# Performance work log

Measured on AMD Instinct MI355X. Metric: run time of the kernel, lower is better.

Reference implementation:

```python
import jax, jax.numpy as jnp
import numpy as np

N_NODES = 50000
N_EDGES = 1600000
DIM_IN = 128
DIM_OUT = 128
EPS = 1e-10


def setup_inputs() -> dict:
    key = jax.random.key(0)
    k1, k2, k3, k4, k5 = jax.random.split(key, 5)
    feat_in = jax.random.normal(k1, (N_NODES, DIM_IN), dtype=jnp.float32)
    rows = jax.random.randint(k2, (N_EDGES,), 0, N_NODES, dtype=jnp.int32)
    cols = jax.random.randint(k3, (N_EDGES,), 0, N_NODES, dtype=jnp.int32)
    # normalized adjacency values (positive, ~1/deg scale)
    vals = jax.random.uniform(k4, (N_EDGES,), dtype=jnp.float32) / 32.0
    W = jax.random.normal(k5, (DIM_OUT, DIM_IN), dtype=jnp.float32) * 0.05
    b = jnp.zeros((DIM_OUT,), dtype=jnp.float32)
    scale = jnp.ones((DIM_OUT,), dtype=jnp.float32)
    offset = jnp.zeros((DIM_OUT,), dtype=jnp.float32)
    return {"feat_in": feat_in, "rows": rows, "cols": cols, "vals": vals,
            "W": W, "b": b, "scale": scale, "offset": offset}


def reference(feat_in, rows, cols, vals, W, b, scale, offset):
    # torch.sparse.mm(adj_norm, feat_in): gather source features, scale by
    # edge value, scatter-add into destination rows.
    msgs = vals[:, None] * feat_in[cols]                       # [E, D_in]
    feat_aggr = jax.ops.segment_sum(msgs, rows, num_segments=N_NODES)  # [N, D_in]
    # f_lin (nn.Linear): x @ W.T + b
    feat_trans = feat_aggr @ W.T + b                           # [N, D_out]
    # act = ReLU
    a = jax.nn.relu(feat_trans)
    # f_norm: per-row (feature-dim) normalization, biased variance
    mean = jnp.mean(a, axis=1, keepdims=True)
    var = jnp.mean((a - mean) ** 2, axis=1, keepdims=True) + EPS
    feat_out = (a - mean) * scale * jax.lax.rsqrt(var) + offset
    return feat_out
```

## Files before the change

kernel.cpp:

```cpp
#include <hip/hip_runtime.h>

typedef unsigned int uint;
typedef unsigned short ushort;
typedef unsigned long long ullong;
typedef __attribute__((ext_vector_type(8))) short short8;
typedef __attribute__((ext_vector_type(4))) float floatx4;

#define N_NODES 50000
#define N_EDGES 1600000
#define DIM 128
#define LN_EPS 1e-10f

#define NB2 1564
#define CAP2 1280
#define EPB 6250
#define SB 256
#define CONVB 256
#define CAPR 76

__device__ __forceinline__ uint f2bf(float x) {
    uint u = __float_as_uint(x);
    return (u + 0x7FFFu + ((u >> 16) & 1u)) >> 16;
}

__global__ __launch_bounds__(1024, 8) void prep(
    const float* __restrict__ feat, const float* __restrict__ W,
    const int* __restrict__ rows, const int* __restrict__ cols,
    const float* __restrict__ vals, int* __restrict__ gcnt,
    int2* __restrict__ perm, uint* __restrict__ featb_u,
    ushort* __restrict__ wbf)
{
    __shared__ int  cnt[NB2];
    __shared__ int  gbase[NB2];
    __shared__ int  lbase[NB2];
    __shared__ int  csum[64];
    __shared__ int2 stageE[EPB];
    const int bx = blockIdx.x;
    const int t  = threadIdx.x;

    if (bx >= SB) {
        const int cb = bx - SB;
        const int stride = CONVB * 1024;
        for (int i = cb * 1024 + t; i < N_NODES * DIM / 4; i += stride) {
            float4 v = ((const float4*)feat)[i];
            ((uint2*)featb_u)[i] = make_uint2(
                f2bf(v.x) | (f2bf(v.y) << 16),
                f2bf(v.z) | (f2bf(v.w) << 16));
        }
        for (int i = cb * 1024 + t; i < DIM * DIM / 4; i += stride) {
            float4 v = ((const float4*)W)[i];
            ushort4 o;
            o.x = (ushort)f2bf(v.x); o.y = (ushort)f2bf(v.y);
            o.z = (ushort)f2bf(v.z); o.w = (ushort)f2bf(v.w);
            ((ushort4*)wbf)[i] = o;
        }
        return;
    }

    for (int i = t; i < NB2; i += 1024) cnt[i] = 0;
    __syncthreads();
    const int base = bx * EPB;
    uint pk[7];
    #pragma unroll
    for (int i = 0; i < 7; ++i) {
        int k = i * 1024 + t;
        if (k < EPB) {
            int r = rows[base + k];
            int rank = atomicAdd(&cnt[r >> 5], 1);
            pk[i] = ((uint)rank << 16) | (uint)r;
        }
    }
    __syncthreads();

    {
        const int rot = (bx * 16) % NB2;
        for (int i = t; i < NB2; i += 1024) {
            int ii = i + rot; if (ii >= NB2) ii -= NB2;
            int c = cnt[ii];
            gbase[ii] = c ? atomicAdd(&gcnt[ii], c) : 0;
        }
    }
    if (t < 64) {
        int s = 0;
        for (int j = 0; j < 25; ++j) {
            int idx = t * 25 + j;
            if (idx < NB2) s += cnt[idx];
        }
        csum[t] = s;
    }
    __syncthreads();
    if (t == 0) {
        int s = 0;
        for (int i = 0; i < 64; ++i) { int c = csum[i]; csum[i] = s; s += c; }
    }
    __syncthreads();
    if (t < 64) {
        int run = csum[t];
        for (int j = 0; j < 25; ++j) {
            int idx = t * 25 + j;
            if (idx < NB2) { lbase[idx] = run; run += cnt[idx]; }
        }
    }
    __syncthreads();

    #pragma unroll
    for (int i = 0; i < 7; ++i) {
        int k = i * 1024 + t;
        if (k < EPB) {
            uint s = pk[i];
            int r = (int)(s & 0xFFFFu);
            int rank = (int)(s >> 16);
            int b = r >> 5;
            int pos = lbase[b] + rank;
            stageE[pos] = make_int2(
                (uint)cols[base + k] | ((uint)(r & 31) << 16) | ((uint)b << 21),
                __float_as_int(vals[base + k]));
        }
    }
    __syncthreads();

    for (int j = t; j < EPB; j += 1024) {
        int2 p = stageE[j];
        uint b = ((uint)p.x) >> 21;
        int pos = gbase[b] + (j - lbase[b]);
        if (pos < CAP2)
            perm[(size_t)b * CAP2 + pos] = p;
    }
}

__global__ __launch_bounds__(512, 8) void agg_fused(
    const int2* __restrict__ perm, const int* __restrict__ gcnt,
    const ushort* __restrict__ featb, const ushort* __restrict__ wbf,
    const float* __restrict__ bias, const float* __restrict__ scale,
    const float* __restrict__ offset, float* __restrict__ out)
{
    __shared__ int2 lists[32 * CAPR];
    ushort* rowsbuf = (ushort*)lists;
    float*  Cbuf    = (float*)lists;
    __shared__ int  lcnt[32];

    const int t = threadIdx.x;

    const int q = NB2 >> 3, rr = NB2 & 7;
    const int xcd = blockIdx.x & 7, within = blockIdx.x >> 3;
    const int hb = (xcd < rr ? xcd * (q + 1) : rr * (q + 1) + (xcd - rr) * q) + within;

    if (t < 32) lcnt[t] = 0;
    __syncthreads();

    int n = gcnt[hb];
    if (n > CAP2) n = CAP2;
    const int2* pb = perm + (size_t)hb * CAP2;

    for (int e = t; e < n; e += 512) {
        ullong pv = __builtin_nontemporal_load((const ullong*)&pb[e]);
        int px = (int)(uint)pv;
        int py = (int)(uint)(pv >> 32);
        int rl = (px >> 16) & 31;
        int pos = atomicAdd(&lcnt[rl], 1);
        if (pos < CAPR)
            lists[rl * CAPR + pos] = make_int2((px & 0xFFFF) << 8, py);
    }
    __syncthreads();

    const int lane = t & 63;
    const int wid  = t >> 6;
    const int rb   = wid * 4;
    const char* fbase = (const char*)featb;
    const uint  lane4 = (uint)lane << 2;

    float ax[4], ay[4];
    #pragma unroll
    for (int j = 0; j < 4; ++j) {
        int rl = rb + j;
        int cnt = lcnt[rl];
        if (cnt > CAPR) cnt = CAPR;
        const int2* L = &lists[rl * CAPR];
        float sx = 0.f, sy = 0.f;
        int e = 0;
        for (; e + 11 < cnt; e += 12) {
            int4 q6[6]; uint g[12];
            #pragma unroll
            for (int k = 0; k < 6; ++k) q6[k] = *(const int4*)&L[e + 2 * k];
            #pragma unroll
            for (int k = 0; k < 6; ++k) {
                g[2*k]   = *(const uint*)(fbase + ((uint)q6[k].x + lane4));
                g[2*k+1] = *(const uint*)(fbase + ((uint)q6[k].z + lane4));
            }
            #pragma unroll
            for (int k = 0; k < 6; ++k) {
                float v0 = __int_as_float(q6[k].y);
                float v1 = __int_as_float(q6[k].w);
                sx = fmaf(v0, __uint_as_float(g[2*k] << 16), sx);
                sy = fmaf(v0, __uint_as_float(g[2*k] & 0xFFFF0000u), sy);
                sx = fmaf(v1, __uint_as_float(g[2*k+1] << 16), sx);
                sy = fmaf(v1, __uint_as_float(g[2*k+1] & 0xFFFF0000u), sy);
            }
        }
        for (; e + 3 < cnt; e += 4) {
            int4 q2[2]; uint g[4];
            #pragma unroll
            for (int k = 0; k < 2; ++k) q2[k] = *(const int4*)&L[e + 2 * k];
            #pragma unroll
            for (int k = 0; k < 2; ++k) {
                g[2*k]   = *(const uint*)(fbase + ((uint)q2[k].x + lane4));
                g[2*k+1] = *(const uint*)(fbase + ((uint)q2[k].z + lane4));
            }
            #pragma unroll
            for (int k = 0; k < 2; ++k) {
                float v0 = __int_as_float(q2[k].y);
                float v1 = __int_as_float(q2[k].w);
                sx = fmaf(v0, __uint_as_float(g[2*k] << 16), sx);
                sy = fmaf(v0, __uint_as_float(g[2*k] & 0xFFFF0000u), sy);
                sx = fmaf(v1, __uint_as_float(g[2*k+1] << 16), sx);
                sy = fmaf(v1, __uint_as_float(g[2*k+1] & 0xFFFF0000u), sy);
            }
        }
        for (; e < cnt; ++e) {
            int2 p = L[e];
            uint g = *(const uint*)(fbase + ((uint)p.x + lane4));
            float v = __int_as_float(p.y);
            sx = fmaf(v, __uint_as_float(g << 16), sx);
            sy = fmaf(v, __uint_as_float(g & 0xFFFF0000u), sy);
        }
        ax[j] = sx; ay[j] = sy;
    }
    __syncthreads();

    #pragma unroll
    for (int j = 0; j < 4; ++j) {
        uint pkd = f2bf(ax[j]) | (f2bf(ay[j]) << 16);
        *(uint*)&rowsbuf[(rb + j) * 136 + 2 * lane] = pkd;
    }
    __syncthreads();

    const int l15  = lane & 15;
    const int quad = lane >> 4;
    const int n0   = wid * 16 + l15;
    const float bb = bias[n0];

    floatx4 acc0 = {0.f, 0.f, 0.f, 0.f};
    floatx4 acc1 = {0.f, 0.f, 0.f, 0.f};
    #pragma unroll
    for (int kt = 0; kt < 4; ++kt) {
        int k0 = kt * 32 + quad * 8;
        short8 af0 = *(const short8*)&rowsbuf[l15 * 136 + k0];
        short8 af1 = *(const short8*)&rowsbuf[(l15 + 16) * 136 + k0];
        short8 bf  = *(const short8*)&wbf[n0 * DIM + k0];
        acc0 = __builtin_amdgcn_mfma_f32_16x16x32_bf16(af0, bf, acc0, 0, 0, 0);
        acc1 = __builtin_amdgcn_mfma_f32_16x16x32_bf16(af1, bf, acc1, 0, 0, 0);
    }
    __syncthreads();

    #pragma unroll
    for (int r = 0; r < 4; ++r) {
        int m = quad * 4 + r;
        Cbuf[m * 132 + n0]        = acc0[r] + bb;
        Cbuf[(m + 16) * 132 + n0] = acc1[r] + bb;
    }
    __syncthreads();

    const float sc0 = scale[lane],  sc1 = scale[lane + 64];
    const float of0 = offset[lane], of1 = offset[lane + 64];

    #pragma unroll
    for (int j = 0; j < 4; ++j) {
        int rl = rb + j;
        int r  = hb * 32 + rl;
        if (r >= N_NODES) continue;
        float A0 = fmaxf(Cbuf[rl * 132 + lane],      0.0f);
        float A1 = fmaxf(Cbuf[rl * 132 + lane + 64], 0.0f);

        float s = A0 + A1;
        #pragma unroll
        for (int off = 32; off >= 1; off >>= 1) s += __shfl_xor(s, off, 64);
        float mean = s * (1.0f / 128.0f);

        float d0 = A0 - mean, d1 = A1 - mean;
        float q2 = d0 * d0 + d1 * d1;
        #pragma unroll
        for (int off = 32; off >= 1; off >>= 1) q2 += __shfl_xor(q2, off, 64);
        float rstd = rsqrtf(q2 * (1.0f / 128.0f) + LN_EPS);

        size_t rowp = (size_t)r * DIM;
        __builtin_nontemporal_store(d0 * sc0 * rstd + of0, &out[rowp + lane]);
        __builtin_nontemporal_store(d1 * sc1 * rstd + of1, &out[rowp + lane + 64]);
    }
}

extern "C" void kernel_launch(void* const* d_in, const int* in_sizes, int n_in,
                              void* d_out, int out_size, void* d_ws, size_t ws_size,
                              hipStream_t stream) {
    const float* feat_in = (const float*)d_in[0];
    const int*   rows    = (const int*)d_in[1];
    const int*   cols    = (const int*)d_in[2];
    const float* vals    = (const float*)d_in[3];
    const float* W       = (const float*)d_in[4];
    const float* bias    = (const float*)d_in[5];
    const float* scale   = (const float*)d_in[6];
    const float* offset  = (const float*)d_in[7];
    float* out = (float*)d_out;

    char* p = (char*)d_ws;
    int2* perm = (int2*)p;                 p += (size_t)NB2 * CAP2 * 8;
    ushort* featb = (ushort*)p;            p += (size_t)N_NODES * DIM * 2;
    ushort* wbf = (ushort*)p;              p += DIM * DIM * 2;
    int*  gcnt = (int*)p;                  p += (size_t)(NB2 + 64) * 4;

    hipMemsetAsync(gcnt, 0, (size_t)NB2 * sizeof(int), stream);

    prep<<<SB + CONVB, 1024, 0, stream>>>(feat_in, W, rows, cols, vals,
                                          gcnt, perm, (uint*)featb, wbf);
    agg_fused<<<NB2, 512, 0, stream>>>(perm, gcnt, featb, wbf,
                                       bias, scale, offset, out);
}
```

Before: 164.2 us.

## Halve aggregation bucket size to 16 rows per block and fold global base into counts

Switches the bucketing from 32 destination rows per bucket to 16, doubling the number of aggregation blocks and halving each block to 256 threads. The GEMM tile is reorganised so each wave computes one 16-row tile against two 16-column slices of W. In prep, the separate gbase array is replaced by storing (global base minus local base) back into the counts array, which saves shared memory and one lookup per edge. The aim is better load balance and occupancy across CUs. In exchange there are more blocks, W fragments are reloaded more often, and per-bucket capacity overflow is more likely with smaller buckets.

```diff
diff --git a/kernel.cpp b/kernel.cpp
--- a/kernel.cpp
+++ b/kernel.cpp
@@ -11,8 +11,8 @@
 #define DIM 128
 #define LN_EPS 1e-10f
 
-#define NB2 1564
-#define CAP2 1280
+#define NB4 3125
+#define CAP4 704
 #define EPB 6250
 #define SB 256
 #define CONVB 256
@@ -30,9 +30,8 @@
     int2* __restrict__ perm, uint* __restrict__ featb_u,
     ushort* __restrict__ wbf)
 {
-    __shared__ int  cnt[NB2];
-    __shared__ int  gbase[NB2];
-    __shared__ int  lbase[NB2];
+    __shared__ int  cnt[NB4];
+    __shared__ int  lbase[NB4];
     __shared__ int  csum[64];
     __shared__ int2 stageE[EPB];
     const int bx = blockIdx.x;
@@ -57,7 +56,7 @@
         return;
     }
 
-    for (int i = t; i < NB2; i += 1024) cnt[i] = 0;
+    for (int i = t; i < NB4; i += 1024) cnt[i] = 0;
     __syncthreads();
     const int base = bx * EPB;
     uint pk[7];
@@ -66,25 +65,28 @@
         int k = i * 1024 + t;
         if (k < EPB) {
             int r = rows[base + k];
-            int rank = atomicAdd(&cnt[r >> 5], 1);
+            int rank = atomicAdd(&cnt[r >> 4], 1);
             pk[i] = ((uint)rank << 16) | (uint)r;
         }
     }
     __syncthreads();
 
-    {
-        const int rot = (bx * 16) % NB2;
-        for (int i = t; i < NB2; i += 1024) {
-            int ii = i + rot; if (ii >= NB2) ii -= NB2;
+    const int rot = (bx * 16) % NB4;
+    int gsav[4];
+    #pragma unroll
+    for (int s = 0; s < 4; ++s) {
+        int i = t + s * 1024;
+        if (i < NB4) {
+            int ii = i + rot; if (ii >= NB4) ii -= NB4;
             int c = cnt[ii];
-            gbase[ii] = c ? atomicAdd(&gcnt[ii], c) : 0;
+            gsav[s] = c ? atomicAdd(&gcnt[ii], c) : 0;
         }
     }
     if (t < 64) {
         int s = 0;
-        for (int j = 0; j < 25; ++j) {
-            int idx = t * 25 + j;
-            if (idx < NB2) s += cnt[idx];
+        for (int j = 0; j < 49; ++j) {
+            int idx = t * 49 + j;
+            if (idx < NB4) s += cnt[idx];
         }
         csum[t] = s;
     }
@@ -96,9 +98,19 @@
     __syncthreads();
     if (t < 64) {
         int run = csum[t];
-        for (int j = 0; j < 25; ++j) {
-            int idx = t * 25 + j;
-            if (idx < NB2) { lbase[idx] = run; run += cnt[idx]; }
+        for (int j = 0; j < 49; ++j) {
+            int idx = t * 49 + j;
+            if (idx < NB4) { lbase[idx] = run; run += cnt[idx]; }
+        }
+    }
+    __syncthreads();
+
+    #pragma unroll
+    for (int s = 0; s < 4; ++s) {
+        int i = t + s * 1024;
+        if (i < NB4) {
+            int ii = i + rot; if (ii >= NB4) ii -= NB4;
+            cnt[ii] = gsav[s] - lbase[ii];
         }
     }
     __syncthreads();
@@ -110,10 +122,10 @@
             uint s = pk[i];
             int r = (int)(s & 0xFFFFu);
             int rank = (int)(s >> 16);
-            int b = r >> 5;
+            int b = r >> 4;
             int pos = lbase[b] + rank;
             stageE[pos] = make_int2(
-                (uint)cols[base + k] | ((uint)(r & 31) << 16) | ((uint)b << 21),
+                (uint)cols[base + k] | ((uint)(r & 15) << 16) | ((uint)b << 20),
                 __float_as_int(vals[base + k]));
         }
     }
@@ -121,42 +133,42 @@
 
     for (int j = t; j < EPB; j += 1024) {
         int2 p = stageE[j];
-        uint b = ((uint)p.x) >> 21;
-        int pos = gbase[b] + (j - lbase[b]);
-        if (pos < CAP2)
-            perm[(size_t)b * CAP2 + pos] = p;
+        uint b = ((uint)p.x) >> 20;
+        int pos = cnt[b] + j;
+        if (pos < CAP4)
+            perm[(size_t)b * CAP4 + pos] = p;
     }
 }
 
-__global__ __launch_bounds__(512, 8) void agg_fused(
+__global__ __launch_bounds__(256, 8) void agg_fused(
     const int2* __restrict__ perm, const int* __restrict__ gcnt,
     const ushort* __restrict__ featb, const ushort* __restrict__ wbf,
     const float* __restrict__ bias, const float* __restrict__ scale,
     const float* __restrict__ offset, float* __restrict__ out)
 {
-    __shared__ int2 lists[32 * CAPR];
+    __shared__ int2 lists[16 * CAPR];
     ushort* rowsbuf = (ushort*)lists;
     float*  Cbuf    = (float*)lists;
-    __shared__ int  lcnt[32];
+    __shared__ int  lcnt[16];
 
     const int t = threadIdx.x;
 
-    const int q = NB2 >> 3, rr = NB2 & 7;
+    const int q = NB4 >> 3, rr = NB4 & 7;
     const int xcd = blockIdx.x & 7, within = blockIdx.x >> 3;
     const int hb = (xcd < rr ? xcd * (q + 1) : rr * (q + 1) + (xcd - rr) * q) + within;
 
-    if (t < 32) lcnt[t] = 0;
+    if (t < 16) lcnt[t] = 0;
     __syncthreads();
 
     int n = gcnt[hb];
-    if (n > CAP2) n = CAP2;
-    const int2* pb = perm + (size_t)hb * CAP2;
-
-    for (int e = t; e < n; e += 512) {
+    if (n > CAP4) n = CAP4;
+    const int2* pb = perm + (size_t)hb * CAP4;
+
+    for (int e = t; e < n; e += 256) {
         ullong pv = __builtin_nontemporal_load((const ullong*)&pb[e]);
         int px = (int)(uint)pv;
         int py = (int)(uint)(pv >> 32);
-        int rl = (px >> 16) & 31;
+        int rl = (px >> 16) & 15;
         int pos = atomicAdd(&lcnt[rl], 1);
         if (pos < CAPR)
             lists[rl * CAPR + pos] = make_int2((px & 0xFFFF) << 8, py);
@@ -236,27 +248,28 @@
 
     const int l15  = lane & 15;
     const int quad = lane >> 4;
-    const int n0   = wid * 16 + l15;
-    const float bb = bias[n0];
-
-    floatx4 acc0 = {0.f, 0.f, 0.f, 0.f};
-    floatx4 acc1 = {0.f, 0.f, 0.f, 0.f};
+    const int n0a  = wid * 32 + l15;
+    const int n0b  = n0a + 16;
+    const float bba = bias[n0a], bbb = bias[n0b];
+
+    floatx4 acca = {0.f, 0.f, 0.f, 0.f};
+    floatx4 accb = {0.f, 0.f, 0.f, 0.f};
     #pragma unroll
     for (int kt = 0; kt < 4; ++kt) {
         int k0 = kt * 32 + quad * 8;
-        short8 af0 = *(const short8*)&rowsbuf[l15 * 136 + k0];
-        short8 af1 = *(const short8*)&rowsbuf[(l15 + 16) * 136 + k0];
-        short8 bf  = *(const short8*)&wbf[n0 * DIM + k0];
-        acc0 = __builtin_amdgcn_mfma_f32_16x16x32_bf16(af0, bf, acc0, 0, 0, 0);
-        acc1 = __builtin_amdgcn_mfma_f32_16x16x32_bf16(af1, bf, acc1, 0, 0, 0);
+        short8 af  = *(const short8*)&rowsbuf[l15 * 136 + k0];
+        short8 bfa = *(const short8*)&wbf[n0a * DIM + k0];
+        short8 bfb = *(const short8*)&wbf[n0b * DIM + k0];
+        acca = __builtin_amdgcn_mfma_f32_16x16x32_bf16(af, bfa, acca, 0, 0, 0);
+        accb = __builtin_amdgcn_mfma_f32_16x16x32_bf16(af, bfb, accb, 0, 0, 0);
     }
     __syncthreads();
 
     #pragma unroll
     for (int r = 0; r < 4; ++r) {
         int m = quad * 4 + r;
-        Cbuf[m * 132 + n0]        = acc0[r] + bb;
-        Cbuf[(m + 16) * 132 + n0] = acc1[r] + bb;
+        Cbuf[m * 132 + n0a] = acca[r] + bba;
+        Cbuf[m * 132 + n0b] = accb[r] + bbb;
     }
     __syncthreads();
 
@@ -266,8 +279,7 @@
     #pragma unroll
     for (int j = 0; j < 4; ++j) {
         int rl = rb + j;
-        int r  = hb * 32 + rl;
-        if (r >= N_NODES) continue;
+        int r  = hb * 16 + rl;
         float A0 = fmaxf(Cbuf[rl * 132 + lane],      0.0f);
         float A1 = fmaxf(Cbuf[rl * 132 + lane + 64], 0.0f);
 
@@ -302,15 +314,15 @@
     float* out = (float*)d_out;
 
     char* p = (char*)d_ws;
-    int2* perm = (int2*)p;                 p += (size_t)NB2 * CAP2 * 8;
+    int2* perm = (int2*)p;                 p += (size_t)NB4 * CAP4 * 8;
     ushort* featb = (ushort*)p;            p += (size_t)N_NODES * DIM * 2;
     ushort* wbf = (ushort*)p;              p += DIM * DIM * 2;
-    int*  gcnt = (int*)p;                  p += (size_t)(NB2 + 64) * 4;
-
-    hipMemsetAsync(gcnt, 0, (size_t)NB2 * sizeof(int), stream);
+    int*  gcnt = (int*)p;                  p += (size_t)(NB4 + 64) * 4;
+
+    hipMemsetAsync(gcnt, 0, (size_t)NB4 * sizeof(int), stream);
 
     prep<<<SB + CONVB, 1024, 0, stream>>>(feat_in, W, rows, cols, vals,
                                           gcnt, perm, (uint*)featb, wbf);
-    agg_fused<<<NB2, 512, 0, stream>>>(perm, gcnt, featb, wbf,
+    agg_fused<<<NB4, 256, 0, stream>>>(perm, gcnt, featb, wbf,
                                        bias, scale, offset, out);
 }
```

Result: slower. 170.2 us (+3.6%).
